# Kernel tuning notes

Measured on AMD Instinct MI355X. Metric: run time of the kernel, lower is better.

Reference implementation:

```python
import jax, jax.numpy as jnp
import numpy as np

N = 50000      # nodes
E = 800000     # edges
F_IN = 256     # input node features
H = 64         # hidden_dim
C = 10         # num_classes
G = 64         # graphs in batch


def setup_inputs() -> dict:
    key = jax.random.key(0)
    ks = jax.random.split(key, 10)
    x = jax.random.normal(ks[0], (N, F_IN), dtype=jnp.float32)
    edge_index = jax.random.randint(ks[1], (2, E), 0, N, dtype=jnp.int64)
    batch = jnp.sort(jax.random.randint(ks[2], (N,), 0, G, dtype=jnp.int64))
    def glorot(k, fan_in, fan_out):
        return jax.random.normal(k, (fan_in, fan_out), dtype=jnp.float32) / jnp.sqrt(jnp.float32(fan_in))
    return {
        "x": x,
        "edge_index": edge_index,
        "batch": batch,
        "W1": glorot(ks[3], F_IN, H), "b1": jnp.zeros((H,), jnp.float32),
        "W2": glorot(ks[4], H, H),    "b2": jnp.zeros((H,), jnp.float32),
        "W3": glorot(ks[5], H, H),    "b3": jnp.zeros((H,), jnp.float32),
        "lin_W": glorot(ks[6], H, C), "lin_b": jnp.zeros((C,), jnp.float32),
    }


def reference(x, edge_index, batch, W1, b1, W2, b2, W3, b3, lin_W, lin_b):
    src, dst = edge_index[0], edge_index[1]
    # GCN normalization with self-loops: deg counts (A + I) in-degree
    deg = jax.ops.segment_sum(jnp.ones((E,), x.dtype), dst, num_segments=N) + 1.0
    dis = jax.lax.rsqrt(deg)                       # deg^{-1/2}, [N]
    edge_norm = dis[src] * dis[dst]                # [E]
    self_norm = dis * dis                          # [N] (self-loop weight)

    def gcn_conv_relu(h, W, b):
        h = h @ W                                  # [N, H]
        msg = h[src] * edge_norm[:, None]          # gather + scale, [E, H]
        agg = jax.ops.segment_sum(msg, dst, num_segments=N)
        agg = agg + h * self_norm[:, None]         # self-loop contribution
        return jax.nn.relu(agg + b)                # dropout is identity in eval

    h = gcn_conv_relu(x, W1, b1)
    h = gcn_conv_relu(h, W2, b2)
    h = gcn_conv_relu(h, W3, b3)

    # global mean pool over graphs
    counts = jax.ops.segment_sum(jnp.ones((N,), h.dtype), batch, num_segments=G)
    pooled = jax.ops.segment_sum(h, batch, num_segments=G) / jnp.maximum(counts, 1.0)[:, None]
    return pooled @ lin_W + lin_b                  # [G, C]
```

## Files before the change

kernel.cpp:

```cpp
#include <hip/hip_runtime.h>

#define N_NODES 50000
#define N_EDGES 800000
#define F_INPUT 256
#define HDIM 64
#define NCLS 10
#define NGRAPH 64

#define BSHIFT 7
#define NBUCK 391
#define SCAP 4096

typedef float f32x4v __attribute__((ext_vector_type(4)));
typedef short bf16x8 __attribute__((ext_vector_type(8)));

union B8U { uint4 q; bf16x8 v; };

__device__ __forceinline__ float bflo(unsigned v) { return __uint_as_float(v << 16); }
__device__ __forceinline__ float bfhi(unsigned v) { return __uint_as_float(v & 0xFFFF0000u); }
__device__ __forceinline__ unsigned f2b2(float a, float b) {
    unsigned x = __float_as_uint(a); x = (x + 0x7FFF + ((x >> 16) & 1)) >> 16;
    unsigned y = __float_as_uint(b); y = (y + 0x7FFF + ((y >> 16) & 1)) >> 16;
    return x | (y << 16);
}

__device__ __forceinline__ void split2(float x0, float x1, unsigned& h, unsigned& l) {
    unsigned u0 = __float_as_uint(x0), u1 = __float_as_uint(x1);
    unsigned m0 = u0 & 0xFFFF0000u, m1 = u1 & 0xFFFF0000u;
    h = (u0 >> 16) | m1;
    float r0 = x0 - __uint_as_float(m0);
    float r1 = x1 - __uint_as_float(m1);
    l = (__float_as_uint(r0) >> 16) | (__float_as_uint(r1) & 0xFFFF0000u);
}

#define ADD8(b, u)                                    \
    b##0 += bflo(u.x); b##1 += bfhi(u.x);             \
    b##2 += bflo(u.y); b##3 += bfhi(u.y);             \
    b##4 += bflo(u.z); b##5 += bfhi(u.z);             \
    b##6 += bflo(u.w); b##7 += bfhi(u.w);

__global__ __launch_bounds__(256) void k_part(const int* __restrict__ src,
                                              const int* __restrict__ dst,
                                              int* __restrict__ bcnt,
                                              int* __restrict__ stage, int E) {
    __shared__ int cnt[NBUCK];
    __shared__ int base[NBUCK];
    const int tid = threadIdx.x;
    const int e0 = blockIdx.x * 4096;
    int pb[16], pv[16];
    for (int t = tid; t < NBUCK; t += 256) cnt[t] = 0;
    __syncthreads();
#pragma unroll
    for (int j = 0; j < 16; ++j) {
        int e = e0 + j * 256 + tid;
        if (e < E) {
            int s = src[e], d = dst[e];
            pb[j] = d >> BSHIFT;
            pv[j] = (s << BSHIFT) | (d & 127);
            atomicAdd(&cnt[pb[j]], 1);
        } else pb[j] = -1;
    }
    __syncthreads();
    for (int t = tid; t < NBUCK; t += 256) {
        int c = cnt[t];
        base[t] = c ? atomicAdd(&bcnt[t], c) : 0;
        cnt[t] = 0;
    }
    __syncthreads();
#pragma unroll
    for (int j = 0; j < 16; ++j) {
        if (pb[j] >= 0) {
            int r = base[pb[j]] + atomicAdd(&cnt[pb[j]], 1);
            if (r < SCAP) stage[pb[j] * SCAP + r] = pv[j];
        }
    }
}

__global__ __launch_bounds__(256) void k_csr(const int* __restrict__ stage,
                                             const int* __restrict__ bcnt,
                                             float* __restrict__ dis,
                                             int4* __restrict__ rng,
                                             int* __restrict__ eadj, int n) {
    __shared__ int cnt[128];
    __shared__ int loc[128];
    __shared__ int lcur[128];
    __shared__ int ebuf[SCAP];
    const int b = blockIdx.x;
    const int tid = threadIdx.x;
    const int n0 = b << BSHIFT;
    const int nn = min(128, n - n0);
    const int sb = b * SCAP;
    const int len = min(bcnt[b], SCAP);
    if (tid < 128) cnt[tid] = 0;
    __syncthreads();
    for (int j = tid; j < len; j += 256) atomicAdd(&cnt[stage[sb + j] & 127], 1);
    __syncthreads();
    if (tid < 128) loc[tid] = cnt[tid];
    __syncthreads();
    for (int d = 1; d < 128; d <<= 1) {
        int x = 0;
        if (tid < 128 && tid >= d) x = loc[tid - d];
        __syncthreads();
        if (tid < 128) loc[tid] += x;
        __syncthreads();
    }
    if (tid < 128) {
        int ex = loc[tid] - cnt[tid];
        if (tid < nn) {
            int dg = cnt[tid];
            float di = rsqrtf((float)(dg + 1));
            dis[n0 + tid] = di;
            rng[n0 + tid] = make_int4(sb + ex, sb + ex + dg, __float_as_int(di), 0);
        }
        lcur[tid] = ex;
    }
    __syncthreads();
    for (int j = tid; j < len; j += 256) {
        int p = stage[sb + j];
        int rk = atomicAdd(&lcur[p & 127], 1);
        ebuf[rk] = p >> BSHIFT;
    }
    __syncthreads();
    for (int j = tid; j < len; j += 256) eadj[sb + j] = ebuf[j];
}

__global__ __launch_bounds__(256) void k_prepZ(const float* __restrict__ W1,
                                               const float* __restrict__ W2,
                                               const float* __restrict__ W3,
                                               uint4* __restrict__ Bf1,
                                               uint4* __restrict__ Bf2,
                                               uint4* __restrict__ Bf3,
                                               int* __restrict__ bcnt,
                                               float* __restrict__ pooled) {
    int s = blockIdx.x * 256 + threadIdx.x;
    for (int j = s; j < NBUCK; j += 3072) bcnt[j] = 0;
    for (int j = s; j < NGRAPH * HDIM; j += 3072) pooled[j] = 0.f;
    const float* W; uint4* out; int local, KS;
    if (s < 2048)      { W = W1; out = Bf1; local = s;        KS = 8; }
    else if (s < 2560) { W = W2; out = Bf2; local = s - 2048; KS = 2; }
    else               { W = W3; out = Bf3; local = s - 2560; KS = 2; }
    const int lane = local & 63;
    const int t    = (local >> 6) & 3;
    const int ks   = local >> 8;
    const int kb   = ks * 32 + ((lane >> 4) << 3);
    const int col  = t * 16 + (lane & 15);
    unsigned h[4], l[4];
#pragma unroll
    for (int j = 0; j < 4; ++j) {
        float x0 = W[(size_t)(kb + 2 * j) * HDIM + col];
        float x1 = W[(size_t)(kb + 2 * j + 1) * HDIM + col];
        split2(x0, x1, h[j], l[j]);
    }
    out[(ks * 4 + t) * 64 + lane]          = make_uint4(h[0], h[1], h[2], h[3]);
    out[((KS + ks) * 4 + t) * 64 + lane]   = make_uint4(l[0], l[1], l[2], l[3]);
}

__global__ __launch_bounds__(256) void k_gemm_mf(const float* __restrict__ A,
                                                 const uint4* __restrict__ Bf,
                                                 const float* __restrict__ dis,
                                                 unsigned short* __restrict__ C,
                                                 int n, int lda, int ktn) {
    const int tid = threadIdx.x;
    const int ln  = tid & 63;
    const int wv  = tid >> 6;
    const int m   = ln & 15;
    const int kg  = ln >> 4;
    const int grow = blockIdx.x * 64 + wv * 16 + m;
    const float* ar = A + (size_t)min(grow, n - 1) * lda + kg * 8;

    f32x4v acc[4];
#pragma unroll
    for (int t = 0; t < 4; ++t)
#pragma unroll
        for (int j = 0; j < 4; ++j) acc[t][j] = 0.0f;

    float4 c0 = *(const float4*)(ar);
    float4 c1 = *(const float4*)(ar + 4);

    for (int ks = 0; ks < ktn; ++ks) {
        const int kn = (ks + 1 < ktn) ? (ks + 1) * 32 : 0;
        float4 p0 = *(const float4*)(ar + kn);
        float4 p1 = *(const float4*)(ar + kn + 4);

        const uint4* bp = Bf + (size_t)ks * 256 + ln;
        const uint4* bq = Bf + (size_t)(ktn + ks) * 256 + ln;
        B8U bh0, bh1, bh2, bh3, bl0, bl1, bl2, bl3;
        bh0.q = bp[0];   bh1.q = bp[64];  bh2.q = bp[128]; bh3.q = bp[192];
        bl0.q = bq[0];   bl1.q = bq[64];  bl2.q = bq[128]; bl3.q = bq[192];

        B8U ah, al;
        split2(c0.x, c0.y, ah.q.x, al.q.x);
        split2(c0.z, c0.w, ah.q.y, al.q.y);
        split2(c1.x, c1.y, ah.q.z, al.q.z);
        split2(c1.z, c1.w, ah.q.w, al.q.w);

        acc[0] = __builtin_amdgcn_mfma_f32_16x16x32_bf16(bh0.v, ah.v, acc[0], 0, 0, 0);
        acc[1] = __builtin_amdgcn_mfma_f32_16x16x32_bf16(bh1.v, ah.v, acc[1], 0, 0, 0);
        acc[2] = __builtin_amdgcn_mfma_f32_16x16x32_bf16(bh2.v, ah.v, acc[2], 0, 0, 0);
        acc[3] = __builtin_amdgcn_mfma_f32_16x16x32_bf16(bh3.v, ah.v, acc[3], 0, 0, 0);
        acc[0] = __builtin_amdgcn_mfma_f32_16x16x32_bf16(bl0.v, ah.v, acc[0], 0, 0, 0);
        acc[1] = __builtin_amdgcn_mfma_f32_16x16x32_bf16(bl1.v, ah.v, acc[1], 0, 0, 0);
        acc[2] = __builtin_amdgcn_mfma_f32_16x16x32_bf16(bl2.v, ah.v, acc[2], 0, 0, 0);
        acc[3] = __builtin_amdgcn_mfma_f32_16x16x32_bf16(bl3.v, ah.v, acc[3], 0, 0, 0);
        acc[0] = __builtin_amdgcn_mfma_f32_16x16x32_bf16(bh0.v, al.v, acc[0], 0, 0, 0);
        acc[1] = __builtin_amdgcn_mfma_f32_16x16x32_bf16(bh1.v, al.v, acc[1], 0, 0, 0);
        acc[2] = __builtin_amdgcn_mfma_f32_16x16x32_bf16(bh2.v, al.v, acc[2], 0, 0, 0);
        acc[3] = __builtin_amdgcn_mfma_f32_16x16x32_bf16(bh3.v, al.v, acc[3], 0, 0, 0);

        c0 = p0; c1 = p1;
    }

    if (grow < n) {
        const float di = dis[grow];
#pragma unroll
        for (int t = 0; t < 4; ++t) {
            uint2 p;
            p.x = f2b2(acc[t][0] * di, acc[t][1] * di);
            p.y = f2b2(acc[t][2] * di, acc[t][3] * di);
            *(uint2*)(C + (size_t)grow * HDIM + t * 16 + kg * 4) = p;
        }
    }
}

__global__ __launch_bounds__(256) void k_fgg(const unsigned short* __restrict__ h,
                                             const int* __restrict__ eadj,
                                             const int4* __restrict__ rng,
                                             const float* __restrict__ bias,
                                             const uint4* __restrict__ Bf,
                                             const float* __restrict__ dis,
                                             unsigned short* __restrict__ out, int n) {
    __shared__ uint4 rl[32 * 8];
    const int tid = threadIdx.x;
    const int i0 = blockIdx.x * 32;
    const int node = tid >> 3;
    const int l8 = tid & 7;
    const int i = i0 + node;
    uint4 o = make_uint4(0u, 0u, 0u, 0u);
    if (i < n) {
        const int q = l8 * 8;
        const int4 r = rng[i];
        int e = r.x; const int e1 = r.y;
        const float di = __int_as_float(r.z);
        float a0 = 0.f, a1 = 0.f, a2 = 0.f, a3 = 0.f, a4 = 0.f, a5 = 0.f, a6 = 0.f, a7 = 0.f;
        float g0 = 0.f, g1 = 0.f, g2 = 0.f, g3 = 0.f, g4 = 0.f, g5 = 0.f, g6 = 0.f, g7 = 0.f;
#pragma unroll 2
        for (; e + 3 < e1; e += 4) {
            int s0 = eadj[e];
            int s1 = eadj[e + 1];
            int s2 = eadj[e + 2];
            int s3 = eadj[e + 3];
            uint4 u0 = *(const uint4*)(h + (size_t)s0 * HDIM + q);
            uint4 u1 = *(const uint4*)(h + (size_t)s1 * HDIM + q);
            uint4 u2 = *(const uint4*)(h + (size_t)s2 * HDIM + q);
            uint4 u3 = *(const uint4*)(h + (size_t)s3 * HDIM + q);
            ADD8(a, u0)
            ADD8(g, u1)
            ADD8(a, u2)
            ADD8(g, u3)
        }
        for (; e < e1; ++e) {
            int s0 = eadj[e];
            uint4 u0 = *(const uint4*)(h + (size_t)s0 * HDIM + q);
            ADD8(a, u0)
        }
        uint4 us = *(const uint4*)(h + (size_t)i * HDIM + q);
        ADD8(a, us)
        a0 += g0; a1 += g1; a2 += g2; a3 += g3;
        a4 += g4; a5 += g5; a6 += g6; a7 += g7;
        float4 bl = *(const float4*)(bias + q);
        float4 bh = *(const float4*)(bias + q + 4);
        a0 = fmaxf(fmaf(a0, di, bl.x), 0.f);
        a1 = fmaxf(fmaf(a1, di, bl.y), 0.f);
        a2 = fmaxf(fmaf(a2, di, bl.z), 0.f);
        a3 = fmaxf(fmaf(a3, di, bl.w), 0.f);
        a4 = fmaxf(fmaf(a4, di, bh.x), 0.f);
        a5 = fmaxf(fmaf(a5, di, bh.y), 0.f);
        a6 = fmaxf(fmaf(a6, di, bh.z), 0.f);
        a7 = fmaxf(fmaf(a7, di, bh.w), 0.f);
        o.x = f2b2(a0, a1); o.y = f2b2(a2, a3);
        o.z = f2b2(a4, a5); o.w = f2b2(a6, a7);
    }
    rl[node * 8 + (l8 ^ (node & 7))] = o;
    __syncthreads();

    const int ln = tid & 63;
    const int wv = tid >> 6;
    const int m  = ln & 15;
    const int kg = ln >> 4;
    const int row = (wv >> 1) * 16 + m;
    const int ct0 = (wv & 1) * 2;
    f32x4v acc0, acc1;
#pragma unroll
    for (int j = 0; j < 4; ++j) { acc0[j] = 0.f; acc1[j] = 0.f; }
#pragma unroll
    for (int ks = 0; ks < 2; ++ks) {
        B8U af;
        af.q = rl[row * 8 + ((ks * 4 + kg) ^ (row & 7))];
        const uint4* bp = Bf + ks * 256 + ln;
        const uint4* bq = Bf + (2 + ks) * 256 + ln;
        B8U bh0, bh1, bl0, bl1;
        bh0.q = bp[ct0 * 64]; bh1.q = bp[(ct0 + 1) * 64];
        bl0.q = bq[ct0 * 64]; bl1.q = bq[(ct0 + 1) * 64];
        acc0 = __builtin_amdgcn_mfma_f32_16x16x32_bf16(bh0.v, af.v, acc0, 0, 0, 0);
        acc1 = __builtin_amdgcn_mfma_f32_16x16x32_bf16(bh1.v, af.v, acc1, 0, 0, 0);
        acc0 = __builtin_amdgcn_mfma_f32_16x16x32_bf16(bl0.v, af.v, acc0, 0, 0, 0);
        acc1 = __builtin_amdgcn_mfma_f32_16x16x32_bf16(bl1.v, af.v, acc1, 0, 0, 0);
    }
    const int grow = i0 + row;
    if (grow < n) {
        const float di = dis[grow];
        uint2 p;
        p.x = f2b2(acc0[0] * di, acc0[1] * di);
        p.y = f2b2(acc0[2] * di, acc0[3] * di);
        *(uint2*)(out + (size_t)grow * HDIM + ct0 * 16 + kg * 4) = p;
        p.x = f2b2(acc1[0] * di, acc1[1] * di);
        p.y = f2b2(acc1[2] * di, acc1[3] * di);
        *(uint2*)(out + (size_t)grow * HDIM + (ct0 + 1) * 16 + kg * 4) = p;
    }
}

__global__ __launch_bounds__(256) void k_gather_pool(const unsigned short* __restrict__ h,
                                                     const int* __restrict__ eadj,
                                                     const int4* __restrict__ rng,
                                                     const float* __restrict__ bias,
                                                     const int* __restrict__ batch,
                                                     float* __restrict__ pooled, int n) {
    __shared__ float sp[NGRAPH][HDIM];
    const int tid = threadIdx.x;
    int t = blockIdx.x * 256 + tid;
    int i = t >> 3;
    const bool valid = (i < n);
    int q = (t & 7) * 8;
    const int i0 = (blockIdx.x * 256) >> 3;
    const int i1 = min(i0 + 32, n);
    const int gmin = batch[min(i0, n - 1)];
    const int gmax = batch[i1 - 1];
    for (int j = tid; j < NGRAPH * HDIM; j += 256) ((float*)sp)[j] = 0.f;
    __syncthreads();
    if (valid) {
        const int4 r = rng[i];
        int e = r.x; const int e1 = r.y;
        const float di = __int_as_float(r.z);
        float a0 = 0.f, a1 = 0.f, a2 = 0.f, a3 = 0.f, a4 = 0.f, a5 = 0.f, a6 = 0.f, a7 = 0.f;
        float g0 = 0.f, g1 = 0.f, g2 = 0.f, g3 = 0.f, g4 = 0.f, g5 = 0.f, g6 = 0.f, g7 = 0.f;
#pragma unroll 2
        for (; e + 3 < e1; e += 4) {
            int s0 = eadj[e];
            int s1 = eadj[e + 1];
            int s2 = eadj[e + 2];
            int s3 = eadj[e + 3];
            uint4 u0 = *(const uint4*)(h + (size_t)s0 * HDIM + q);
            uint4 u1 = *(const uint4*)(h + (size_t)s1 * HDIM + q);
            uint4 u2 = *(const uint4*)(h + (size_t)s2 * HDIM + q);
            uint4 u3 = *(const uint4*)(h + (size_t)s3 * HDIM + q);
            ADD8(a, u0)
            ADD8(g, u1)
            ADD8(a, u2)
            ADD8(g, u3)
        }
        for (; e < e1; ++e) {
            int s0 = eadj[e];
            uint4 u0 = *(const uint4*)(h + (size_t)s0 * HDIM + q);
            ADD8(a, u0)
        }
        uint4 us = *(const uint4*)(h + (size_t)i * HDIM + q);
        ADD8(a, us)
        a0 += g0; a1 += g1; a2 += g2; a3 += g3;
        a4 += g4; a5 += g5; a6 += g6; a7 += g7;
        float4 bl = *(const float4*)(bias + q);
        float4 bh = *(const float4*)(bias + q + 4);
        a0 = fmaxf(fmaf(a0, di, bl.x), 0.f);
        a1 = fmaxf(fmaf(a1, di, bl.y), 0.f);
        a2 = fmaxf(fmaf(a2, di, bl.z), 0.f);
        a3 = fmaxf(fmaf(a3, di, bl.w), 0.f);
        a4 = fmaxf(fmaf(a4, di, bh.x), 0.f);
        a5 = fmaxf(fmaf(a5, di, bh.y), 0.f);
        a6 = fmaxf(fmaf(a6, di, bh.z), 0.f);
        a7 = fmaxf(fmaf(a7, di, bh.w), 0.f);
        int g = batch[i];
        atomicAdd(&sp[g][q + 0], a0); atomicAdd(&sp[g][q + 1], a1);
        atomicAdd(&sp[g][q + 2], a2); atomicAdd(&sp[g][q + 3], a3);
        atomicAdd(&sp[g][q + 4], a4); atomicAdd(&sp[g][q + 5], a5);
        atomicAdd(&sp[g][q + 6], a6); atomicAdd(&sp[g][q + 7], a7);
    }
    __syncthreads();
    int rows = gmax - gmin + 1;
    for (int j = tid; j < rows * HDIM; j += 256) {
        int r = j >> 6, c = j & 63;
        float v = sp[gmin + r][c];
        if (v != 0.f) atomicAdd(&pooled[(gmin + r) * HDIM + c], v);
    }
}

__global__ __launch_bounds__(640) void k_head(const float* __restrict__ pooled,
                                              const int* __restrict__ batch,
                                              const float* __restrict__ linW,
                                              const float* __restrict__ linb,
                                              float* __restrict__ out, int n) {
    int t = threadIdx.x;
    if (t >= NGRAPH * NCLS) return;
    int g = t / NCLS;
    int c = t - g * NCLS;
    int lo = 0, hi = n;
    while (lo < hi) { int m = (lo + hi) >> 1; if (batch[m] < g) lo = m + 1; else hi = m; }
    int s = lo;
    lo = 0; hi = n;
    while (lo < hi) { int m = (lo + hi) >> 1; if (batch[m] < g + 1) lo = m + 1; else hi = m; }
    float inv = 1.0f / fmaxf((float)(lo - s), 1.0f);
    float acc = linb[c];
#pragma unroll
    for (int k = 0; k < HDIM; ++k)
        acc = fmaf(pooled[g * HDIM + k] * inv, linW[k * NCLS + c], acc);
    out[g * NCLS + c] = acc;
}

extern "C" void kernel_launch(void* const* d_in, const int* in_sizes, int n_in,
                              void* d_out, int out_size, void* d_ws, size_t ws_size,
                              hipStream_t stream) {
    (void)in_sizes; (void)n_in; (void)out_size; (void)ws_size;
    const float* x    = (const float*)d_in[0];
    const int*   ei   = (const int*)d_in[1];
    const int*   batch= (const int*)d_in[2];
    const float* W1   = (const float*)d_in[3];
    const float* b1   = (const float*)d_in[4];
    const float* W2   = (const float*)d_in[5];
    const float* b2   = (const float*)d_in[6];
    const float* W3   = (const float*)d_in[7];
    const float* b3   = (const float*)d_in[8];
    const float* linW = (const float*)d_in[9];
    const float* linb = (const float*)d_in[10];
    float* out = (float*)d_out;

    const int N = N_NODES, E = N_EDGES;
    const int* src = ei;
    const int* dst = ei + E;

    char* ws = (char*)d_ws;
    unsigned short* hA = (unsigned short*)ws; ws += (size_t)N * HDIM * 2;
    unsigned short* hB = (unsigned short*)ws; ws += (size_t)N * HDIM * 2;
    float* dis    = (float*)ws; ws += (size_t)N * 4;
    int*   eadj   = (int*)ws;   ws += (size_t)NBUCK * SCAP * 4;
    int*   stage  = (int*)ws;   ws += (size_t)NBUCK * SCAP * 4;
    int4*  rng    = (int4*)ws;  ws += (size_t)N * 16;
    int*   bcnt   = (int*)ws;   ws += ((size_t)NBUCK * 4 + 15) & ~(size_t)15;
    float* pooled = (float*)ws; ws += (size_t)NGRAPH * HDIM * 4;
    uint4* Bf1    = (uint4*)ws; ws += (size_t)2 * 8 * 4 * 64 * 16;
    uint4* Bf2    = (uint4*)ws; ws += (size_t)2 * 2 * 4 * 64 * 16;
    uint4* Bf3    = (uint4*)ws; ws += (size_t)2 * 2 * 4 * 64 * 16;

    const int nbE = (E + 4095) / 4096;
    const int gb  = (N + 63) / 64;
    const int nF  = (N + 31) / 32;

    k_prepZ<<<12, 256, 0, stream>>>(W1, W2, W3, Bf1, Bf2, Bf3, bcnt, pooled);
    k_part<<<nbE, 256, 0, stream>>>(src, dst, bcnt, stage, E);
    k_csr<<<NBUCK, 256, 0, stream>>>(stage, bcnt, dis, rng, eadj, N);

    k_gemm_mf<<<gb, 256, 0, stream>>>(x, Bf1, dis, hA, N, F_INPUT, 8);
    k_fgg<<<nF, 256, 0, stream>>>(hA, eadj, rng, b1, Bf2, dis, hB, N);
    k_fgg<<<nF, 256, 0, stream>>>(hB, eadj, rng, b2, Bf3, dis, hA, N);
    k_gather_pool<<<nF, 256, 0, stream>>>(hA, eadj, rng, b3, batch, pooled, N);
    k_head<<<1, 640, 0, stream>>>(pooled, batch, linW, linb, out, N);
}
```

Before: 226.9 us.

## Overlap edge partitioning with layer-1 GEMM and fuse head into pooling

Merges the edge-bucketing kernel and the first feature GEMM into one launch, with the first blocks partitioning edges and the rest computing x@W1. Because dis is not ready yet, the GEMM output is left unscaled and a new first-layer gather kernel applies the per-edge dis[src]*dis[dst] weights itself. The classifier head is folded into the pooling kernel through a last-block-done atomic counter. This removes two launches and lets the independent partition and GEMM work run concurrently, at the cost of an extra dis load per edge in layer 1 and a grid-wide completion counter.

```diff
diff --git a/kernel.cpp b/kernel.cpp
--- a/kernel.cpp
+++ b/kernel.cpp
@@ -10,6 +10,7 @@
 #define BSHIFT 7
 #define NBUCK 391
 #define SCAP 4096
+#define PARTB 196
 
 typedef float f32x4v __attribute__((ext_vector_type(4)));
 typedef short bf16x8 __attribute__((ext_vector_type(8)));
@@ -39,39 +40,141 @@
     b##4 += bflo(u.z); b##5 += bfhi(u.z);             \
     b##6 += bflo(u.w); b##7 += bfhi(u.w);
 
-__global__ __launch_bounds__(256) void k_part(const int* __restrict__ src,
-                                              const int* __restrict__ dst,
-                                              int* __restrict__ bcnt,
-                                              int* __restrict__ stage, int E) {
+#define FMA8(b, u, wt)                                                  \
+    b##0 = fmaf(bflo(u.x), wt, b##0); b##1 = fmaf(bfhi(u.x), wt, b##1); \
+    b##2 = fmaf(bflo(u.y), wt, b##2); b##3 = fmaf(bfhi(u.y), wt, b##3); \
+    b##4 = fmaf(bflo(u.z), wt, b##4); b##5 = fmaf(bfhi(u.z), wt, b##5); \
+    b##6 = fmaf(bflo(u.w), wt, b##6); b##7 = fmaf(bfhi(u.w), wt, b##7);
+
+__global__ __launch_bounds__(256) void k_prepZ(const float* __restrict__ W1,
+                                               const float* __restrict__ W2,
+                                               const float* __restrict__ W3,
+                                               uint4* __restrict__ Bf1,
+                                               uint4* __restrict__ Bf2,
+                                               uint4* __restrict__ Bf3,
+                                               int* __restrict__ bcnt,
+                                               float* __restrict__ pooled) {
+    int s = blockIdx.x * 256 + threadIdx.x;
+    for (int j = s; j < NBUCK + 1; j += 3072) bcnt[j] = 0;
+    for (int j = s; j < NGRAPH * HDIM; j += 3072) pooled[j] = 0.f;
+    const float* W; uint4* out; int local, KS;
+    if (s < 2048)      { W = W1; out = Bf1; local = s;        KS = 8; }
+    else if (s < 2560) { W = W2; out = Bf2; local = s - 2048; KS = 2; }
+    else               { W = W3; out = Bf3; local = s - 2560; KS = 2; }
+    const int lane = local & 63;
+    const int t    = (local >> 6) & 3;
+    const int ks   = local >> 8;
+    const int kb   = ks * 32 + ((lane >> 4) << 3);
+    const int col  = t * 16 + (lane & 15);
+    unsigned h[4], l[4];
+#pragma unroll
+    for (int j = 0; j < 4; ++j) {
+        float x0 = W[(size_t)(kb + 2 * j) * HDIM + col];
+        float x1 = W[(size_t)(kb + 2 * j + 1) * HDIM + col];
+        split2(x0, x1, h[j], l[j]);
+    }
+    out[(ks * 4 + t) * 64 + lane]          = make_uint4(h[0], h[1], h[2], h[3]);
+    out[((KS + ks) * 4 + t) * 64 + lane]   = make_uint4(l[0], l[1], l[2], l[3]);
+}
+
+__global__ __launch_bounds__(256) void k_pg(const int* __restrict__ src,
+                                            const int* __restrict__ dst,
+                                            int* __restrict__ bcnt,
+                                            int* __restrict__ stage, int E,
+                                            const float* __restrict__ A,
+                                            const uint4* __restrict__ Bf,
+                                            unsigned short* __restrict__ C,
+                                            int n, int lda, int ktn) {
     __shared__ int cnt[NBUCK];
     __shared__ int base[NBUCK];
     const int tid = threadIdx.x;
-    const int e0 = blockIdx.x * 4096;
-    int pb[16], pv[16];
-    for (int t = tid; t < NBUCK; t += 256) cnt[t] = 0;
-    __syncthreads();
-#pragma unroll
-    for (int j = 0; j < 16; ++j) {
-        int e = e0 + j * 256 + tid;
-        if (e < E) {
-            int s = src[e], d = dst[e];
-            pb[j] = d >> BSHIFT;
-            pv[j] = (s << BSHIFT) | (d & 127);
-            atomicAdd(&cnt[pb[j]], 1);
-        } else pb[j] = -1;
-    }
-    __syncthreads();
-    for (int t = tid; t < NBUCK; t += 256) {
-        int c = cnt[t];
-        base[t] = c ? atomicAdd(&bcnt[t], c) : 0;
-        cnt[t] = 0;
-    }
-    __syncthreads();
-#pragma unroll
-    for (int j = 0; j < 16; ++j) {
-        if (pb[j] >= 0) {
-            int r = base[pb[j]] + atomicAdd(&cnt[pb[j]], 1);
-            if (r < SCAP) stage[pb[j] * SCAP + r] = pv[j];
+    if ((int)blockIdx.x < PARTB) {
+        const int e0 = blockIdx.x * 4096;
+        int pb[16], pv[16];
+        for (int t = tid; t < NBUCK; t += 256) cnt[t] = 0;
+        __syncthreads();
+#pragma unroll
+        for (int j = 0; j < 16; ++j) {
+            int e = e0 + j * 256 + tid;
+            if (e < E) {
+                int s = src[e], d = dst[e];
+                pb[j] = d >> BSHIFT;
+                pv[j] = (s << BSHIFT) | (d & 127);
+                atomicAdd(&cnt[pb[j]], 1);
+            } else pb[j] = -1;
+        }
+        __syncthreads();
+        for (int t = tid; t < NBUCK; t += 256) {
+            int c = cnt[t];
+            base[t] = c ? atomicAdd(&bcnt[t], c) : 0;
+            cnt[t] = 0;
+        }
+        __syncthreads();
+#pragma unroll
+        for (int j = 0; j < 16; ++j) {
+            if (pb[j] >= 0) {
+                int r = base[pb[j]] + atomicAdd(&cnt[pb[j]], 1);
+                if (r < SCAP) stage[pb[j] * SCAP + r] = pv[j];
+            }
+        }
+        return;
+    }
+    const int ln  = tid & 63;
+    const int wv  = tid >> 6;
+    const int m   = ln & 15;
+    const int kg  = ln >> 4;
+    const int grow = (blockIdx.x - PARTB) * 64 + wv * 16 + m;
+    const float* ar = A + (size_t)min(grow, n - 1) * lda + kg * 8;
+
+    f32x4v acc[4];
+#pragma unroll
+    for (int t = 0; t < 4; ++t)
+#pragma unroll
+        for (int j = 0; j < 4; ++j) acc[t][j] = 0.0f;
+
+    float4 c0 = *(const float4*)(ar);
+    float4 c1 = *(const float4*)(ar + 4);
+
+    for (int ks = 0; ks < ktn; ++ks) {
+        const int kn = (ks + 1 < ktn) ? (ks + 1) * 32 : 0;
+        float4 p0 = *(const float4*)(ar + kn);
+        float4 p1 = *(const float4*)(ar + kn + 4);
+
+        const uint4* bp = Bf + (size_t)ks * 256 + ln;
+        const uint4* bq = Bf + (size_t)(ktn + ks) * 256 + ln;
+        B8U bh0, bh1, bh2, bh3, bl0, bl1, bl2, bl3;
+        bh0.q = bp[0];   bh1.q = bp[64];  bh2.q = bp[128]; bh3.q = bp[192];
+        bl0.q = bq[0];   bl1.q = bq[64];  bl2.q = bq[128]; bl3.q = bq[192];
+
+        B8U ah, al;
+        split2(c0.x, c0.y, ah.q.x, al.q.x);
+        split2(c0.z, c0.w, ah.q.y, al.q.y);
+        split2(c1.x, c1.y, ah.q.z, al.q.z);
+        split2(c1.z, c1.w, ah.q.w, al.q.w);
+
+        acc[0] = __builtin_amdgcn_mfma_f32_16x16x32_bf16(bh0.v, ah.v, acc[0], 0, 0, 0);
+        acc[1] = __builtin_amdgcn_mfma_f32_16x16x32_bf16(bh1.v, ah.v, acc[1], 0, 0, 0);
+        acc[2] = __builtin_amdgcn_mfma_f32_16x16x32_bf16(bh2.v, ah.v, acc[2], 0, 0, 0);
+        acc[3] = __builtin_amdgcn_mfma_f32_16x16x32_bf16(bh3.v, ah.v, acc[3], 0, 0, 0);
+        acc[0] = __builtin_amdgcn_mfma_f32_16x16x32_bf16(bl0.v, ah.v, acc[0], 0, 0, 0);
+        acc[1] = __builtin_amdgcn_mfma_f32_16x16x32_bf16(bl1.v, ah.v, acc[1], 0, 0, 0);
+        acc[2] = __builtin_amdgcn_mfma_f32_16x16x32_bf16(bl2.v, ah.v, acc[2], 0, 0, 0);
+        acc[3] = __builtin_amdgcn_mfma_f32_16x16x32_bf16(bl3.v, ah.v, acc[3], 0, 0, 0);
+        acc[0] = __builtin_amdgcn_mfma_f32_16x16x32_bf16(bh0.v, al.v, acc[0], 0, 0, 0);
+        acc[1] = __builtin_amdgcn_mfma_f32_16x16x32_bf16(bh1.v, al.v, acc[1], 0, 0, 0);
+        acc[2] = __builtin_amdgcn_mfma_f32_16x16x32_bf16(bh2.v, al.v, acc[2], 0, 0, 0);
+        acc[3] = __builtin_amdgcn_mfma_f32_16x16x32_bf16(bh3.v, al.v, acc[3], 0, 0, 0);
+
+        c0 = p0; c1 = p1;
+    }
+
+    if (grow < n) {
+#pragma unroll
+        for (int t = 0; t < 4; ++t) {
+            uint2 p;
+            p.x = f2b2(acc[t][0], acc[t][1]);
+            p.y = f2b2(acc[t][2], acc[t][3]);
+            *(uint2*)(C + (size_t)grow * HDIM + t * 16 + kg * 4) = p;
         }
     }
 }
@@ -124,101 +227,102 @@
     for (int j = tid; j < len; j += 256) eadj[sb + j] = ebuf[j];
 }
 
-__global__ __launch_bounds__(256) void k_prepZ(const float* __restrict__ W1,
-                                               const float* __restrict__ W2,
-                                               const float* __restrict__ W3,
-                                               uint4* __restrict__ Bf1,
-                                               uint4* __restrict__ Bf2,
-                                               uint4* __restrict__ Bf3,
-                                               int* __restrict__ bcnt,
-                                               float* __restrict__ pooled) {
-    int s = blockIdx.x * 256 + threadIdx.x;
-    for (int j = s; j < NBUCK; j += 3072) bcnt[j] = 0;
-    for (int j = s; j < NGRAPH * HDIM; j += 3072) pooled[j] = 0.f;
-    const float* W; uint4* out; int local, KS;
-    if (s < 2048)      { W = W1; out = Bf1; local = s;        KS = 8; }
-    else if (s < 2560) { W = W2; out = Bf2; local = s - 2048; KS = 2; }
-    else               { W = W3; out = Bf3; local = s - 2560; KS = 2; }
-    const int lane = local & 63;
-    const int t    = (local >> 6) & 3;
-    const int ks   = local >> 8;
-    const int kb   = ks * 32 + ((lane >> 4) << 3);
-    const int col  = t * 16 + (lane & 15);
-    unsigned h[4], l[4];
-#pragma unroll
-    for (int j = 0; j < 4; ++j) {
-        float x0 = W[(size_t)(kb + 2 * j) * HDIM + col];
-        float x1 = W[(size_t)(kb + 2 * j + 1) * HDIM + col];
-        split2(x0, x1, h[j], l[j]);
-    }
-    out[(ks * 4 + t) * 64 + lane]          = make_uint4(h[0], h[1], h[2], h[3]);
-    out[((KS + ks) * 4 + t) * 64 + lane]   = make_uint4(l[0], l[1], l[2], l[3]);
-}
-
-__global__ __launch_bounds__(256) void k_gemm_mf(const float* __restrict__ A,
-                                                 const uint4* __restrict__ Bf,
-                                                 const float* __restrict__ dis,
-                                                 unsigned short* __restrict__ C,
-                                                 int n, int lda, int ktn) {
+__global__ __launch_bounds__(256) void k_fggw(const unsigned short* __restrict__ h,
+                                              const int* __restrict__ eadj,
+                                              const int4* __restrict__ rng,
+                                              const float* __restrict__ dis,
+                                              const float* __restrict__ bias,
+                                              const uint4* __restrict__ Bf,
+                                              unsigned short* __restrict__ out, int n) {
+    __shared__ uint4 rl[32 * 8];
     const int tid = threadIdx.x;
-    const int ln  = tid & 63;
-    const int wv  = tid >> 6;
-    const int m   = ln & 15;
-    const int kg  = ln >> 4;
-    const int grow = blockIdx.x * 64 + wv * 16 + m;
-    const float* ar = A + (size_t)min(grow, n - 1) * lda + kg * 8;
-
-    f32x4v acc[4];
-#pragma unroll
-    for (int t = 0; t < 4; ++t)
-#pragma unroll
-        for (int j = 0; j < 4; ++j) acc[t][j] = 0.0f;
-
-    float4 c0 = *(const float4*)(ar);
-    float4 c1 = *(const float4*)(ar + 4);
-
-    for (int ks = 0; ks < ktn; ++ks) {
-        const int kn = (ks + 1 < ktn) ? (ks + 1) * 32 : 0;
-        float4 p0 = *(const float4*)(ar + kn);
-        float4 p1 = *(const float4*)(ar + kn + 4);
-
-        const uint4* bp = Bf + (size_t)ks * 256 + ln;
-        const uint4* bq = Bf + (size_t)(ktn + ks) * 256 + ln;
-        B8U bh0, bh1, bh2, bh3, bl0, bl1, bl2, bl3;
-        bh0.q = bp[0];   bh1.q = bp[64];  bh2.q = bp[128]; bh3.q = bp[192];
-        bl0.q = bq[0];   bl1.q = bq[64];  bl2.q = bq[128]; bl3.q = bq[192];
-
-        B8U ah, al;
-        split2(c0.x, c0.y, ah.q.x, al.q.x);
-        split2(c0.z, c0.w, ah.q.y, al.q.y);
-        split2(c1.x, c1.y, ah.q.z, al.q.z);
-        split2(c1.z, c1.w, ah.q.w, al.q.w);
-
-        acc[0] = __builtin_amdgcn_mfma_f32_16x16x32_bf16(bh0.v, ah.v, acc[0], 0, 0, 0);
-        acc[1] = __builtin_amdgcn_mfma_f32_16x16x32_bf16(bh1.v, ah.v, acc[1], 0, 0, 0);
-        acc[2] = __builtin_amdgcn_mfma_f32_16x16x32_bf16(bh2.v, ah.v, acc[2], 0, 0, 0);
-        acc[3] = __builtin_amdgcn_mfma_f32_16x16x32_bf16(bh3.v, ah.v, acc[3], 0, 0, 0);
-        acc[0] = __builtin_amdgcn_mfma_f32_16x16x32_bf16(bl0.v, ah.v, acc[0], 0, 0, 0);
-        acc[1] = __builtin_amdgcn_mfma_f32_16x16x32_bf16(bl1.v, ah.v, acc[1], 0, 0, 0);
-        acc[2] = __builtin_amdgcn_mfma_f32_16x16x32_bf16(bl2.v, ah.v, acc[2], 0, 0, 0);
-        acc[3] = __builtin_amdgcn_mfma_f32_16x16x32_bf16(bl3.v, ah.v, acc[3], 0, 0, 0);
-        acc[0] = __builtin_amdgcn_mfma_f32_16x16x32_bf16(bh0.v, al.v, acc[0], 0, 0, 0);
-        acc[1] = __builtin_amdgcn_mfma_f32_16x16x32_bf16(bh1.v, al.v, acc[1], 0, 0, 0);
-        acc[2] = __builtin_amdgcn_mfma_f32_16x16x32_bf16(bh2.v, al.v, acc[2], 0, 0, 0);
-        acc[3] = __builtin_amdgcn_mfma_f32_16x16x32_bf16(bh3.v, al.v, acc[3], 0, 0, 0);
-
-        c0 = p0; c1 = p1;
-    }
-
+    const int i0 = blockIdx.x * 32;
+    const int node = tid >> 3;
+    const int l8 = tid & 7;
+    const int i = i0 + node;
+    uint4 o = make_uint4(0u, 0u, 0u, 0u);
+    if (i < n) {
+        const int q = l8 * 8;
+        const int4 r = rng[i];
+        int e = r.x; const int e1 = r.y;
+        const float di = __int_as_float(r.z);
+        float a0 = 0.f, a1 = 0.f, a2 = 0.f, a3 = 0.f, a4 = 0.f, a5 = 0.f, a6 = 0.f, a7 = 0.f;
+        float g0 = 0.f, g1 = 0.f, g2 = 0.f, g3 = 0.f, g4 = 0.f, g5 = 0.f, g6 = 0.f, g7 = 0.f;
+#pragma unroll 2
+        for (; e + 3 < e1; e += 4) {
+            int s0 = eadj[e];
+            int s1 = eadj[e + 1];
+            int s2 = eadj[e + 2];
+            int s3 = eadj[e + 3];
+            uint4 u0 = *(const uint4*)(h + (size_t)s0 * HDIM + q);
+            uint4 u1 = *(const uint4*)(h + (size_t)s1 * HDIM + q);
+            uint4 u2 = *(const uint4*)(h + (size_t)s2 * HDIM + q);
+            uint4 u3 = *(const uint4*)(h + (size_t)s3 * HDIM + q);
+            float w0 = dis[s0] * di;
+            float w1 = dis[s1] * di;
+            float w2 = dis[s2] * di;
+            float w3 = dis[s3] * di;
+            FMA8(a, u0, w0)
+            FMA8(g, u1, w1)
+            FMA8(a, u2, w2)
+            FMA8(g, u3, w3)
+        }
+        for (; e < e1; ++e) {
+            int s0 = eadj[e];
+            uint4 u0 = *(const uint4*)(h + (size_t)s0 * HDIM + q);
+            float w0 = dis[s0] * di;
+            FMA8(a, u0, w0)
+        }
+        uint4 us = *(const uint4*)(h + (size_t)i * HDIM + q);
+        float sn = di * di;
+        FMA8(a, us, sn)
+        a0 += g0; a1 += g1; a2 += g2; a3 += g3;
+        a4 += g4; a5 += g5; a6 += g6; a7 += g7;
+        float4 bl = *(const float4*)(bias + q);
+        float4 bh = *(const float4*)(bias + q + 4);
+        a0 = fmaxf(a0 + bl.x, 0.f); a1 = fmaxf(a1 + bl.y, 0.f);
+        a2 = fmaxf(a2 + bl.z, 0.f); a3 = fmaxf(a3 + bl.w, 0.f);
+        a4 = fmaxf(a4 + bh.x, 0.f); a5 = fmaxf(a5 + bh.y, 0.f);
+        a6 = fmaxf(a6 + bh.z, 0.f); a7 = fmaxf(a7 + bh.w, 0.f);
+        o.x = f2b2(a0, a1); o.y = f2b2(a2, a3);
+        o.z = f2b2(a4, a5); o.w = f2b2(a6, a7);
+    }
+    rl[node * 8 + (l8 ^ (node & 7))] = o;
+    __syncthreads();
+
+    const int ln = tid & 63;
+    const int wv = tid >> 6;
+    const int m  = ln & 15;
+    const int kg = ln >> 4;
+    const int row = (wv >> 1) * 16 + m;
+    const int ct0 = (wv & 1) * 2;
+    f32x4v acc0, acc1;
+#pragma unroll
+    for (int j = 0; j < 4; ++j) { acc0[j] = 0.f; acc1[j] = 0.f; }
+#pragma unroll
+    for (int ks = 0; ks < 2; ++ks) {
+        B8U af;
+        af.q = rl[row * 8 + ((ks * 4 + kg) ^ (row & 7))];
+        const uint4* bp = Bf + ks * 256 + ln;
+        const uint4* bq = Bf + (2 + ks) * 256 + ln;
+        B8U bh0, bh1, bl0, bl1;
+        bh0.q = bp[ct0 * 64]; bh1.q = bp[(ct0 + 1) * 64];
+        bl0.q = bq[ct0 * 64]; bl1.q = bq[(ct0 + 1) * 64];
+        acc0 = __builtin_amdgcn_mfma_f32_16x16x32_bf16(bh0.v, af.v, acc0, 0, 0, 0);
+        acc1 = __builtin_amdgcn_mfma_f32_16x16x32_bf16(bh1.v, af.v, acc1, 0, 0, 0);
+        acc0 = __builtin_amdgcn_mfma_f32_16x16x32_bf16(bl0.v, af.v, acc0, 0, 0, 0);
+        acc1 = __builtin_amdgcn_mfma_f32_16x16x32_bf16(bl1.v, af.v, acc1, 0, 0, 0);
+    }
+    const int grow = i0 + row;
     if (grow < n) {
         const float di = dis[grow];
-#pragma unroll
-        for (int t = 0; t < 4; ++t) {
-            uint2 p;
-            p.x = f2b2(acc[t][0] * di, acc[t][1] * di);
-            p.y = f2b2(acc[t][2] * di, acc[t][3] * di);
-            *(uint2*)(C + (size_t)grow * HDIM + t * 16 + kg * 4) = p;
-        }
+        uint2 p;
+        p.x = f2b2(acc0[0] * di, acc0[1] * di);
+        p.y = f2b2(acc0[2] * di, acc0[3] * di);
+        *(uint2*)(out + (size_t)grow * HDIM + ct0 * 16 + kg * 4) = p;
+        p.x = f2b2(acc1[0] * di, acc1[1] * di);
+        p.y = f2b2(acc1[2] * di, acc1[3] * di);
+        *(uint2*)(out + (size_t)grow * HDIM + (ct0 + 1) * 16 + kg * 4) = p;
     }
 }
 
@@ -319,13 +423,18 @@
     }
 }
 
-__global__ __launch_bounds__(256) void k_gather_pool(const unsigned short* __restrict__ h,
-                                                     const int* __restrict__ eadj,
-                                                     const int4* __restrict__ rng,
-                                                     const float* __restrict__ bias,
-                                                     const int* __restrict__ batch,
-                                                     float* __restrict__ pooled, int n) {
+__global__ __launch_bounds__(256) void k_gpool_head(const unsigned short* __restrict__ h,
+                                                    const int* __restrict__ eadj,
+                                                    const int4* __restrict__ rng,
+                                                    const float* __restrict__ bias,
+                                                    const int* __restrict__ batch,
+                                                    float* __restrict__ pooled,
+                                                    int* __restrict__ pcnt,
+                                                    const float* __restrict__ linW,
+                                                    const float* __restrict__ linb,
+                                                    float* __restrict__ out, int n) {
     __shared__ float sp[NGRAPH][HDIM];
+    __shared__ int lastf;
     const int tid = threadIdx.x;
     int t = blockIdx.x * 256 + tid;
     int i = t >> 3;
@@ -390,28 +499,28 @@
         float v = sp[gmin + r][c];
         if (v != 0.f) atomicAdd(&pooled[(gmin + r) * HDIM + c], v);
     }
-}
-
-__global__ __launch_bounds__(640) void k_head(const float* __restrict__ pooled,
-                                              const int* __restrict__ batch,
-                                              const float* __restrict__ linW,
-                                              const float* __restrict__ linb,
-                                              float* __restrict__ out, int n) {
-    int t = threadIdx.x;
-    if (t >= NGRAPH * NCLS) return;
-    int g = t / NCLS;
-    int c = t - g * NCLS;
-    int lo = 0, hi = n;
-    while (lo < hi) { int m = (lo + hi) >> 1; if (batch[m] < g) lo = m + 1; else hi = m; }
-    int s = lo;
-    lo = 0; hi = n;
-    while (lo < hi) { int m = (lo + hi) >> 1; if (batch[m] < g + 1) lo = m + 1; else hi = m; }
-    float inv = 1.0f / fmaxf((float)(lo - s), 1.0f);
-    float acc = linb[c];
-#pragma unroll
-    for (int k = 0; k < HDIM; ++k)
-        acc = fmaf(pooled[g * HDIM + k] * inv, linW[k * NCLS + c], acc);
-    out[g * NCLS + c] = acc;
+    __syncthreads();
+    __threadfence();
+    if (tid == 0) lastf = (atomicAdd(pcnt, 1) == (int)gridDim.x - 1);
+    __syncthreads();
+    if (lastf) {
+        __threadfence();
+        for (int tt = tid; tt < NGRAPH * NCLS; tt += 256) {
+            int g = tt / NCLS;
+            int c = tt - g * NCLS;
+            int lo = 0, hi = n;
+            while (lo < hi) { int m2 = (lo + hi) >> 1; if (batch[m2] < g) lo = m2 + 1; else hi = m2; }
+            int s = lo;
+            lo = 0; hi = n;
+            while (lo < hi) { int m2 = (lo + hi) >> 1; if (batch[m2] < g + 1) lo = m2 + 1; else hi = m2; }
+            float inv = 1.0f / fmaxf((float)(lo - s), 1.0f);
+            float acc = linb[c];
+#pragma unroll
+            for (int k = 0; k < HDIM; ++k)
+                acc = fmaf(pooled[g * HDIM + k] * inv, linW[k * NCLS + c], acc);
+            out[g * NCLS + c] = acc;
+        }
+    }
 }
 
 extern "C" void kernel_launch(void* const* d_in, const int* in_sizes, int n_in,
@@ -442,23 +551,22 @@
     int*   eadj   = (int*)ws;   ws += (size_t)NBUCK * SCAP * 4;
     int*   stage  = (int*)ws;   ws += (size_t)NBUCK * SCAP * 4;
     int4*  rng    = (int4*)ws;  ws += (size_t)N * 16;
-    int*   bcnt   = (int*)ws;   ws += ((size_t)NBUCK * 4 + 15) & ~(size_t)15;
+    int*   bcnt   = (int*)ws;   ws += ((size_t)(NBUCK + 1) * 4 + 15) & ~(size_t)15;
     float* pooled = (float*)ws; ws += (size_t)NGRAPH * HDIM * 4;
     uint4* Bf1    = (uint4*)ws; ws += (size_t)2 * 8 * 4 * 64 * 16;
     uint4* Bf2    = (uint4*)ws; ws += (size_t)2 * 2 * 4 * 64 * 16;
     uint4* Bf3    = (uint4*)ws; ws += (size_t)2 * 2 * 4 * 64 * 16;
-
-    const int nbE = (E + 4095) / 4096;
+    int* pcnt = bcnt + NBUCK;
+
     const int gb  = (N + 63) / 64;
     const int nF  = (N + 31) / 32;
 
     k_prepZ<<<12, 256, 0, stream>>>(W1, W2, W3, Bf1, Bf2, Bf3, bcnt, pooled);
-    k_part<<<nbE, 256, 0, stream>>>(src, dst, bcnt, stage, E);
+    k_pg<<<PARTB + gb, 256, 0, stream>>>(src, dst, bcnt, stage, E,
+                                         x, Bf1, hA, N, F_INPUT, 8);
     k_csr<<<NBUCK, 256, 0, stream>>>(stage, bcnt, dis, rng, eadj, N);
-
-    k_gemm_mf<<<gb, 256, 0, stream>>>(x, Bf1, dis, hA, N, F_INPUT, 8);
-    k_fgg<<<nF, 256, 0, stream>>>(hA, eadj, rng, b1, Bf2, dis, hB, N);
+    k_fggw<<<nF, 256, 0, stream>>>(hA, eadj, rng, dis, b1, Bf2, hB, N);
     k_fgg<<<nF, 256, 0, stream>>>(hB, eadj, rng, b2, Bf3, dis, hA, N);
-    k_gather_pool<<<nF, 256, 0, stream>>>(hA, eadj, rng, b3, batch, pooled, N);
-    k_head<<<1, 640, 0, stream>>>(pooled, batch, linW, linb, out, N);
-}
+    k_gpool_head<<<nF, 256, 0, stream>>>(hA, eadj, rng, b3, batch, pooled, pcnt,
+                                         linW, linb, out, N);
+}
```

Result: slower. 303.8 us (+33.9%).
